# Performance work log

Measured on AMD Instinct MI355X. Metric: run time of the kernel, lower is better.

## Reference

```python
import jax, jax.numpy as jnp
import numpy as np

N_NODES = 50000


def gcn_conv(x, W, b, row, col, num_nodes):
    """PyG-style GCNConv: out = D^{-1/2}(A+I)D^{-1/2} (x @ W) + b.

    row/col already include self-loops. x: [N, Fin], W: [Fin, Fout].
    """
    h = x @ W  # [N, Fout]
    deg = jax.ops.segment_sum(jnp.ones_like(col, dtype=h.dtype), col,
                              num_segments=num_nodes)  # in-degree incl. self-loop
    dinv = jnp.where(deg > 0, jax.lax.rsqrt(deg), 0.0)
    norm = dinv[row] * dinv[col]  # [E]
    msgs = h[row] * norm[:, None]  # gather + scale, [E, Fout]
    out = jax.ops.segment_sum(msgs, col, num_segments=num_nodes)  # scatter-add
    return out + b


def setup_inputs() -> dict:
    key = jax.random.key(0)
    k1, k2, k3, k4 = jax.random.split(key, 4)
    Fin, Fh, Fout = 128, 128, 64
    E = 800000
    x = jax.random.normal(k1, (N_NODES, Fin), dtype=jnp.float32)
    edge_index = jax.random.randint(k2, (2, E), 0, N_NODES, dtype=jnp.int64)
    # Glorot-ish init for weights
    W1 = jax.random.normal(k3, (Fin, Fh), dtype=jnp.float32) / np.sqrt(Fin)
    b1 = jnp.zeros((Fh,), dtype=jnp.float32)
    W2 = jax.random.normal(k4, (Fh, Fout), dtype=jnp.float32) / np.sqrt(Fh)
    b2 = jnp.zeros((Fout,), dtype=jnp.float32)
    return {"x": x, "edge_index": edge_index, "W1": W1, "b1": b1,
            "W2": W2, "b2": b2}


def reference(x, edge_index, W1, b1, W2, b2):
    n = x.shape[0]
    # add self-loops once (shared by both conv layers)
    loops = jnp.arange(n, dtype=edge_index.dtype)
    row = jnp.concatenate([edge_index[0], loops])
    col = jnp.concatenate([edge_index[1], loops])
    h = jax.nn.relu(gcn_conv(x, W1, b1, row, col, n))
    # dropout(p=0.5) is identity in eval mode (self.training == False)
    return gcn_conv(h, W2, b2, row, col, n)
```

## Files before the change

### kernel.cpp

```cpp
#include <hip/hip_runtime.h>


constexpr int KD = 128;
constexpr int CHUNK = 2048;
constexpr int BCAP = 6144;

using short8  = __attribute__((ext_vector_type(8))) short;
using float4v = __attribute__((ext_vector_type(4))) float;
using uint4v  = __attribute__((ext_vector_type(4))) unsigned int;


__device__ __forceinline__ unsigned short f2bf(float f) {
    unsigned int u = __float_as_uint(f);
    u = (u + 0x7fffu + ((u >> 16) & 1u)) >> 16;
    return (unsigned short)u;
}

__device__ __forceinline__ float2 bfpair(unsigned int u) {
    float2 f;
    f.x = __uint_as_float(u << 16);
    f.y = __uint_as_float(u & 0xffff0000u);
    return f;
}

__device__ __forceinline__ unsigned int packbf(float x, float y) {
    return (unsigned int)f2bf(x) | ((unsigned int)f2bf(y) << 16);
}

__device__ __forceinline__ void bfsplit(float x, unsigned short& h, unsigned short& l) {
    h = f2bf(x);
    float fh = __uint_as_float((unsigned int)h << 16);
    l = f2bf(x - fh);
}

__global__ __launch_bounds__(256) void scatter_setup(
        const int* __restrict__ row, const int* __restrict__ col,
        int* gcur, unsigned int* __restrict__ bpack, int E, int NBS,
        const float* __restrict__ W1, unsigned short* __restrict__ Wth1,
        unsigned short* __restrict__ Wtl1,
        const float* __restrict__ W2, unsigned short* __restrict__ Wth2,
        unsigned short* __restrict__ Wtl2) {
    __shared__ int lh[256];
    __shared__ int lbase[256];

    if ((int)blockIdx.x >= NBS) {
        int id = ((int)blockIdx.x - NBS) * 256 + threadIdx.x;
        unsigned short h, l;
        if (id < 16384) {
            int k = id >> 7, n = id & 127;
            bfsplit(W1[id], h, l);
            Wth1[n * KD + k] = h;
            Wtl1[n * KD + k] = l;
        } else {
            int id2 = id - 16384;
            int k = id2 >> 6, n = id2 & 63;
            bfsplit(W2[id2], h, l);
            Wth2[n * KD + k] = h;
            Wtl2[n * KD + k] = l;
        }
        return;
    }

    lh[threadIdx.x] = 0;
    __syncthreads();
    int base = (int)blockIdx.x * CHUNK;
#pragma unroll
    for (int r = 0; r < CHUNK / 256; ++r) {
        int e = base + r * 256 + threadIdx.x;
        if (e < E) atomicAdd(&lh[col[e] >> 8], 1);
    }
    __syncthreads();
    int c0 = lh[threadIdx.x];
    lbase[threadIdx.x] = c0 ? (threadIdx.x * BCAP + atomicAdd(&gcur[threadIdx.x], c0)) : 0;
    __syncthreads();
    lh[threadIdx.x] = 0;
    __syncthreads();
#pragma unroll
    for (int r = 0; r < CHUNK / 256; ++r) {
        int e = base + r * 256 + threadIdx.x;
        if (e < E) {
            int c = col[e];
            int b = c >> 8;
            int slot = lbase[b] + atomicAdd(&lh[b], 1);
            bpack[slot] = ((unsigned int)row[e] << 16) | (unsigned int)c;
        }
    }
}

__global__ __launch_bounds__(256) void csr_and_gemm1(
        const unsigned int* __restrict__ bpack, const int* __restrict__ gcur,
        int* __restrict__ rowptrS, float* __restrict__ dinv,
        unsigned short* __restrict__ srow, int N, int E, int NBUCKET,
        const float* __restrict__ X,
        const unsigned short* __restrict__ Wth,
        const unsigned short* __restrict__ Wtl,
        unsigned short* __restrict__ G) {
    __shared__ int s[256];
    __shared__ int lh[1024];
    __shared__ int lcur[1024];
    __shared__ int sh_bstart;

    if ((int)blockIdx.x < NBUCKET) {
        int b = blockIdx.x;
        int t = threadIdx.x;
        int cntb = gcur[t];
        s[t] = cntb;
        __syncthreads();
        for (int off = 1; off < 256; off <<= 1) {
            int tv = (t >= off) ? s[t - off] : 0;
            __syncthreads();
            s[t] += tv;
            __syncthreads();
        }
        if (t == b) sh_bstart = s[t] - cntb;
        if (b == 0 && t == 0) rowptrS[4 * N] = E;
#pragma unroll
        for (int k = 0; k < 4; ++k) lh[t * 4 + k] = 0;
        __syncthreads();
        int bstart = sh_bstart;
        int nE = gcur[b];
        int base = b * BCAP;
        for (int i = t; i < nE; i += 256) {
            unsigned int p = bpack[base + i];
            atomicAdd(&lh[(p & 255) * 4 + (p >> 30)], 1);
        }
        __syncthreads();
        int e0 = lh[t * 4], e1 = lh[t * 4 + 1], e2 = lh[t * 4 + 2], e3 = lh[t * 4 + 3];
        int v = e0 + e1 + e2 + e3;
        s[t] = v;
        __syncthreads();
        for (int off = 1; off < 256; off <<= 1) {
            int tv = (t >= off) ? s[t - off] : 0;
            __syncthreads();
            s[t] += tv;
            __syncthreads();
        }
        int myStart = bstart + s[t] - v;
        int node = (b << 8) + t;
        if (node < N) {
            rowptrS[node * 4 + 0] = myStart;
            rowptrS[node * 4 + 1] = myStart + e0;
            rowptrS[node * 4 + 2] = myStart + e0 + e1;
            rowptrS[node * 4 + 3] = myStart + e0 + e1 + e2;
            dinv[node] = rsqrtf(1.0f + (float)v);
        }
        lcur[t * 4 + 0] = myStart;
        lcur[t * 4 + 1] = myStart + e0;
        lcur[t * 4 + 2] = myStart + e0 + e1;
        lcur[t * 4 + 3] = myStart + e0 + e1 + e2;
        __syncthreads();
        for (int i = t; i < nE; i += 256) {
            unsigned int p = bpack[base + i];
            int slot = atomicAdd(&lcur[(p & 255) * 4 + (p >> 30)], 1);
            srow[slot] = (unsigned short)(p >> 16);
        }
    } else {
        constexpr int FOUT = 128, NT = 8;
        int wave = threadIdx.x >> 6;
        int lane = threadIdx.x & 63;
        int row0 = (((int)blockIdx.x - NBUCKET) * 4 + wave) * 16;
        if (row0 >= N) return;
        int m = lane & 15;
        int quad = lane >> 4;

        float4v acc[NT];
#pragma unroll
        for (int ct = 0; ct < NT; ++ct) acc[ct] = (float4v){0.f, 0.f, 0.f, 0.f};

        const float* xrow = X + (size_t)(row0 + m) * KD + quad * 8;

#pragma unroll
        for (int ks = 0; ks < 4; ++ks) {
            float4 xa = *(const float4*)(xrow + ks * 32);
            float4 xb = *(const float4*)(xrow + ks * 32 + 4);
            float xs[8] = {xa.x, xa.y, xa.z, xa.w, xb.x, xb.y, xb.z, xb.w};
            short8 ah, al;
#pragma unroll
            for (int j = 0; j < 8; ++j) {
                unsigned short h, l;
                bfsplit(xs[j], h, l);
                ah[j] = (short)h;
                al[j] = (short)l;
            }
            int koff = ks * 32 + quad * 8;
#pragma unroll
            for (int ct = 0; ct < NT; ++ct) {
                short8 bh = *(const short8*)(Wth + (size_t)(ct * 16 + m) * KD + koff);
                short8 bl = *(const short8*)(Wtl + (size_t)(ct * 16 + m) * KD + koff);
                acc[ct] = __builtin_amdgcn_mfma_f32_16x16x32_bf16(ah, bh, acc[ct], 0, 0, 0);
                acc[ct] = __builtin_amdgcn_mfma_f32_16x16x32_bf16(al, bh, acc[ct], 0, 0, 0);
                acc[ct] = __builtin_amdgcn_mfma_f32_16x16x32_bf16(ah, bl, acc[ct], 0, 0, 0);
            }
        }

#pragma unroll
        for (int r = 0; r < 4; ++r) {
            int row = row0 + quad * 4 + r;
#pragma unroll
            for (int ct = 0; ct < NT; ++ct) {
                G[(size_t)row * FOUT + ct * 16 + m] = f2bf(acc[ct][r]);
            }
        }
    }
}

__global__ __launch_bounds__(256) void gather128_gemm2(
        const int* __restrict__ rowptrS,
        const unsigned short* __restrict__ srow,
        const unsigned int* __restrict__ G,
        const float* __restrict__ dinv,
        const float* __restrict__ bias,
        const unsigned short* __restrict__ Wth,
        const unsigned short* __restrict__ Wtl,
        unsigned short* __restrict__ G2,
        int N, int E) {
    __shared__ unsigned int lhs[16 * 64];
    __shared__ float ldinv[16];

    int lane = threadIdx.x & 63;
    int l16 = threadIdx.x & 15;
    int q = threadIdx.x >> 4;
    int node = (int)blockIdx.x * 16 + q;
    bool valid = node < N;
    int nc = valid ? node : 0;
    int beg = rowptrS[nc * 4];
    int end = rowptrS[nc * 4 + 4];
    int deg = valid ? (end - beg) : 0;
    float dn = dinv[nc];
    if (l16 == 0) ldinv[q] = dn;

    const uint4v* Gv = (const uint4v*)G;

    uint4v s0 = Gv[(size_t)nc * 16 + l16];
    float ac[8];
    {
        float2 v0 = bfpair(s0[0]), v1 = bfpair(s0[1]);
        float2 v2 = bfpair(s0[2]), v3 = bfpair(s0[3]);
        ac[0] = v0.x * dn; ac[1] = v0.y * dn;
        ac[2] = v1.x * dn; ac[3] = v1.y * dn;
        ac[4] = v2.x * dn; ac[5] = v2.y * dn;
        ac[6] = v3.x * dn; ac[7] = v3.y * dn;
    }

    int dm = max(deg, __shfl_xor(deg, 16));
    dm = max(dm, __shfl_xor(dm, 32));

    for (int w = 0; w < dm; w += 16) {
        int li = w + l16;
        li = (li < deg) ? li : (deg > 0 ? deg - 1 : 0);
        li += beg;
        li = (li < E) ? li : (E - 1);
        int rv = (int)srow[li];
        float dv = dinv[rv];
        int lim = dm - w;
        for (int g = 0; g < 16 && g < lim; g += 8) {
            uint4v u[8];
            float dr[8];
#pragma unroll
            for (int j = 0; j < 8; ++j) {
                int src = (lane & 48) | (g + j);
                int r = __shfl(rv, src);
                dr[j] = __shfl(dv, src);
                u[j] = Gv[(size_t)r * 16 + l16];
            }
            float sa[8] = {0.f, 0.f, 0.f, 0.f, 0.f, 0.f, 0.f, 0.f};
#pragma unroll
            for (int j = 0; j < 8; ++j) {
                bool ok = (w + g + j) < deg;
#pragma unroll
                for (int c = 0; c < 4; ++c) {
                    unsigned int uv = ok ? u[j][c] : 0u;
                    float2 v = bfpair(uv);
                    sa[2 * c]     = fmaf(dr[j], v.x, sa[2 * c]);
                    sa[2 * c + 1] = fmaf(dr[j], v.y, sa[2 * c + 1]);
                }
            }
#pragma unroll
            for (int c = 0; c < 8; ++c) ac[c] += sa[c];
        }
    }

    {
        float4 bv0 = ((const float4*)bias)[l16 * 2];
        float4 bv1 = ((const float4*)bias)[l16 * 2 + 1];
        float o[8];
        o[0] = ac[0] * dn + bv0.x; o[1] = ac[1] * dn + bv0.y;
        o[2] = ac[2] * dn + bv0.z; o[3] = ac[3] * dn + bv0.w;
        o[4] = ac[4] * dn + bv1.x; o[5] = ac[5] * dn + bv1.y;
        o[6] = ac[6] * dn + bv1.z; o[7] = ac[7] * dn + bv1.w;
#pragma unroll
        for (int c = 0; c < 8; ++c) o[c] = fmaxf(o[c], 0.f);
        int lb = q * 64 + l16 * 4;
        lhs[lb + 0] = packbf(o[0], o[1]);
        lhs[lb + 1] = packbf(o[2], o[3]);
        lhs[lb + 2] = packbf(o[4], o[5]);
        lhs[lb + 3] = packbf(o[6], o[7]);
    }
    __syncthreads();

    int ct = threadIdx.x >> 6;
    int m = lane & 15;
    int quad = lane >> 4;

    float4v acc = (float4v){0.f, 0.f, 0.f, 0.f};
#pragma unroll
    for (int ks = 0; ks < 4; ++ks) {
        short8 a = *(const short8*)&lhs[m * 64 + ks * 16 + quad * 4];
        int koff = ks * 32 + quad * 8;
        short8 bh = *(const short8*)(Wth + (size_t)(ct * 16 + m) * KD + koff);
        short8 bl = *(const short8*)(Wtl + (size_t)(ct * 16 + m) * KD + koff);
        acc = __builtin_amdgcn_mfma_f32_16x16x32_bf16(a, bh, acc, 0, 0, 0);
        acc = __builtin_amdgcn_mfma_f32_16x16x32_bf16(a, bl, acc, 0, 0, 0);
    }

#pragma unroll
    for (int r = 0; r < 4; ++r) {
        int rr = quad * 4 + r;
        int gnode = (int)blockIdx.x * 16 + rr;
        if (gnode < N) {
            G2[(size_t)gnode * 64 + ct * 16 + m] = f2bf(acc[r] * ldinv[rr]);
        }
    }
}

template <bool RELU>
__global__ __launch_bounds__(256) void gather64(const int* __restrict__ rowptrS,
                                                const unsigned short* __restrict__ srow,
                                                const unsigned int* __restrict__ G,
                                                const float* __restrict__ dinv,
                                                const float* __restrict__ bias,
                                                float* __restrict__ O, int N, int E) {
    int tid = blockIdx.x * 256 + (int)threadIdx.x;
    int node = tid >> 4;
    int lane = threadIdx.x & 63;
    int l16 = lane & 15;
    bool valid = node < N;
    int nc = valid ? node : (N - 1);
    int beg = rowptrS[nc * 4];
    int end = rowptrS[nc * 4 + 4];
    int deg = valid ? (end - beg) : 0;

    uint2 s0 = ((const uint2*)G)[(size_t)nc * 16 + l16];
    float2 p0 = bfpair(s0.x), p1 = bfpair(s0.y);
    float ax = p0.x, ay = p0.y, az = p1.x, aw = p1.y;

    int dm = max(deg, __shfl_xor(deg, 16));
    dm = max(dm, __shfl_xor(dm, 32));

    for (int w = 0; w < dm; w += 16) {
        int li = w + l16;
        li = (li < deg) ? li : (deg > 0 ? deg - 1 : 0);
        li += beg;
        li = (li < E) ? li : (E - 1);
        int rv = (int)srow[li];
        int lim = dm - w;
        for (int g = 0; g < 16 && g < lim; g += 8) {
            uint2 u[8];
#pragma unroll
            for (int j = 0; j < 8; ++j) {
                int src = (lane & 48) | (g + j);
                int r = __shfl(rv, src);
                u[j] = ((const uint2*)G)[(size_t)r * 16 + l16];
            }
            float sx = 0.f, sy = 0.f, sz = 0.f, sw = 0.f;
#pragma unroll
            for (int j = 0; j < 8; ++j) {
                bool ok = (w + g + j) < deg;
                unsigned int ux = ok ? u[j].x : 0u;
                unsigned int uy = ok ? u[j].y : 0u;
                float2 v0 = bfpair(ux), v1 = bfpair(uy);
                sx += v0.x; sy += v0.y; sz += v1.x; sw += v1.y;
            }
            ax += sx; ay += sy; az += sz; aw += sw;
        }
    }
    if (!valid) return;
    float s = dinv[nc];
    float4 bv = ((const float4*)bias)[l16];
    float ox = ax * s + bv.x;
    float oy = ay * s + bv.y;
    float oz = az * s + bv.z;
    float ow = aw * s + bv.w;
    if (RELU) {
        ox = fmaxf(ox, 0.f); oy = fmaxf(oy, 0.f);
        oz = fmaxf(oz, 0.f); ow = fmaxf(ow, 0.f);
    }
    float4v o = {ox, oy, oz, ow};
    __builtin_nontemporal_store(o, (float4v*)O + (size_t)nc * 16 + l16);
}

extern "C" void kernel_launch(void* const* d_in, const int* in_sizes, int n_in,
                              void* d_out, int out_size, void* d_ws, size_t ws_size,
                              hipStream_t stream) {
    const float* x  = (const float*)d_in[0];
    const int*   ei = (const int*)d_in[1];
    const float* W1 = (const float*)d_in[2];
    const float* b1 = (const float*)d_in[3];
    const float* W2 = (const float*)d_in[4];
    const float* b2 = (const float*)d_in[5];
    float* out = (float*)d_out;

    int N = in_sizes[0] / 128;
    int E = in_sizes[1] / 2;
    const int* row = ei;
    const int* col = ei + E;

    char* ws = (char*)d_ws;
    float* dinv    = (float*)(ws + 0x000000);
    int*   rowptrS = (int*)  (ws + 0x080000);
    int*   gcur    = (int*)  (ws + 0x150000);
    unsigned short* srow = (unsigned short*)(ws + 0x160000);
    unsigned short* g1 = (unsigned short*)(ws + 0x440000);
    unsigned short* wth1 = (unsigned short*)(ws + 0x10C0000);
    unsigned short* wtl1 = (unsigned short*)(ws + 0x10D0000);
    unsigned short* wth2 = (unsigned short*)(ws + 0x10E0000);
    unsigned short* wtl2 = (unsigned short*)(ws + 0x10F0000);
    unsigned int* bpack = (unsigned int*)(ws + 0x1200000);
    unsigned short* g2 = (unsigned short*)(ws + 0x2C00000);

    int NB_BKT  = (E + CHUNK - 1) / CHUNK;
    int NBUCKET = (N + 255) / 256;
    int NB_GEMM1 = (N + 63) / 64;
    int NB_SETUP = 96;

    hipMemsetAsync(gcur, 0, 256 * sizeof(int), stream);
    scatter_setup<<<NB_BKT + NB_SETUP, 256, 0, stream>>>(
        row, col, gcur, bpack, E, NB_BKT, W1, wth1, wtl1, W2, wth2, wtl2);
    csr_and_gemm1<<<NBUCKET + NB_GEMM1, 256, 0, stream>>>(
        bpack, gcur, rowptrS, dinv, srow, N, E, NBUCKET, x, wth1, wtl1, g1);

    int nb;
    nb = (N + 15) / 16;
    gather128_gemm2<<<nb, 256, 0, stream>>>(rowptrS, srow, (const unsigned int*)g1,
                                            dinv, b1, wth2, wtl2, g2, N, E);

    nb = (N + 15) / 16;
    gather64<false><<<nb, 256, 0, stream>>>(rowptrS, srow, (const unsigned int*)g2,
                                            dinv, b2, out, N, E);
}
```

Before: 183.4 us.

## Fuse all GCN stages into one cooperative persistent kernel with grid syncs

Replaces the memset and four separate kernel launches with one cooperative kernel of 1024 persistent blocks. The blocks loop over the virtual block ranges of each stage, with grid.sync between stages. This removes per-launch overhead and the inter-kernel gaps, but adds grid-wide barrier cost and a fixed grid size that may limit occupancy or load balance. The old multi-launch path is kept as a fallback if the cooperative launch fails.

```diff
diff --git a/kernel.cpp b/kernel.cpp
--- a/kernel.cpp
+++ b/kernel.cpp
@@ -1,9 +1,13 @@
 #include <hip/hip_runtime.h>
+#include <hip/hip_cooperative_groups.h>
+
+namespace cg = cooperative_groups;
 
 
 constexpr int KD = 128;
 constexpr int CHUNK = 2048;
 constexpr int BCAP = 6144;
+constexpr int GRID_COOP = 1024;
 
 using short8  = __attribute__((ext_vector_type(8))) short;
 using float4v = __attribute__((ext_vector_type(4))) float;
@@ -32,6 +36,358 @@
     float fh = __uint_as_float((unsigned int)h << 16);
     l = f2bf(x - fh);
 }
+
+struct KP {
+    const int* row; const int* col;
+    const float* X; const float* W1; const float* b1;
+    const float* W2; const float* b2;
+    float* out;
+    int* gcur; unsigned int* bpack; int* rowptrS; float* dinv;
+    unsigned short* srow; unsigned short* g1;
+    unsigned short* wth1; unsigned short* wtl1;
+    unsigned short* wth2; unsigned short* wtl2;
+    unsigned short* g2;
+    int N, E, NBS, NB1, NBUCKET, NB2, NB3, NB4;
+};
+
+__global__ __launch_bounds__(256, 4) void gcn_fused(KP p) {
+    cg::grid_group grid = cg::this_grid();
+
+    __shared__ int s_s[256];
+    __shared__ int s_lh[1024];
+    __shared__ int s_lcur[1024];
+    __shared__ int s_b;
+    __shared__ unsigned int s_lhs[16 * 64];
+    __shared__ float s_ldinv[16];
+
+    const int t = threadIdx.x;
+    const int lane = t & 63;
+
+    if (blockIdx.x == 0) p.gcur[t] = 0;
+    grid.sync();
+
+    for (int vb = blockIdx.x; vb < p.NB1; vb += gridDim.x) {
+        if (vb >= p.NBS) {
+            int id = (vb - p.NBS) * 256 + t;
+            unsigned short h, l;
+            if (id < 16384) {
+                int k = id >> 7, n = id & 127;
+                bfsplit(p.W1[id], h, l);
+                p.wth1[n * KD + k] = h;
+                p.wtl1[n * KD + k] = l;
+            } else {
+                int id2 = id - 16384;
+                int k = id2 >> 6, n = id2 & 63;
+                bfsplit(p.W2[id2], h, l);
+                p.wth2[n * KD + k] = h;
+                p.wtl2[n * KD + k] = l;
+            }
+        } else {
+            int* lh = s_lh;
+            int* lbase = s_lcur;
+            lh[t] = 0;
+            __syncthreads();
+            int base = vb * CHUNK;
+#pragma unroll
+            for (int r = 0; r < CHUNK / 256; ++r) {
+                int e = base + r * 256 + t;
+                if (e < p.E) atomicAdd(&lh[p.col[e] >> 8], 1);
+            }
+            __syncthreads();
+            int c0 = lh[t];
+            lbase[t] = c0 ? (t * BCAP + atomicAdd(&p.gcur[t], c0)) : 0;
+            __syncthreads();
+            lh[t] = 0;
+            __syncthreads();
+#pragma unroll
+            for (int r = 0; r < CHUNK / 256; ++r) {
+                int e = base + r * 256 + t;
+                if (e < p.E) {
+                    int c = p.col[e];
+                    int b = c >> 8;
+                    int slot = lbase[b] + atomicAdd(&lh[b], 1);
+                    p.bpack[slot] = ((unsigned int)p.row[e] << 16) | (unsigned int)c;
+                }
+            }
+            __syncthreads();
+        }
+    }
+    grid.sync();
+
+    for (int vb = blockIdx.x; vb < p.NB2; vb += gridDim.x) {
+        if (vb < p.NBUCKET) {
+            int b = vb;
+            int cntb = p.gcur[t];
+            s_s[t] = cntb;
+            __syncthreads();
+            for (int off = 1; off < 256; off <<= 1) {
+                int tv = (t >= off) ? s_s[t - off] : 0;
+                __syncthreads();
+                s_s[t] += tv;
+                __syncthreads();
+            }
+            if (t == b) s_b = s_s[t] - cntb;
+            if (b == 0 && t == 0) p.rowptrS[4 * p.N] = p.E;
+#pragma unroll
+            for (int k = 0; k < 4; ++k) s_lh[t * 4 + k] = 0;
+            __syncthreads();
+            int bstart = s_b;
+            int nE = p.gcur[b];
+            int base = b * BCAP;
+            for (int i = t; i < nE; i += 256) {
+                unsigned int pk = p.bpack[base + i];
+                atomicAdd(&s_lh[(pk & 255) * 4 + (pk >> 30)], 1);
+            }
+            __syncthreads();
+            int e0 = s_lh[t * 4], e1 = s_lh[t * 4 + 1];
+            int e2 = s_lh[t * 4 + 2], e3 = s_lh[t * 4 + 3];
+            int v = e0 + e1 + e2 + e3;
+            s_s[t] = v;
+            __syncthreads();
+            for (int off = 1; off < 256; off <<= 1) {
+                int tv = (t >= off) ? s_s[t - off] : 0;
+                __syncthreads();
+                s_s[t] += tv;
+                __syncthreads();
+            }
+            int myStart = bstart + s_s[t] - v;
+            int node = (b << 8) + t;
+            if (node < p.N) {
+                p.rowptrS[node * 4 + 0] = myStart;
+                p.rowptrS[node * 4 + 1] = myStart + e0;
+                p.rowptrS[node * 4 + 2] = myStart + e0 + e1;
+                p.rowptrS[node * 4 + 3] = myStart + e0 + e1 + e2;
+                p.dinv[node] = rsqrtf(1.0f + (float)v);
+            }
+            s_lcur[t * 4 + 0] = myStart;
+            s_lcur[t * 4 + 1] = myStart + e0;
+            s_lcur[t * 4 + 2] = myStart + e0 + e1;
+            s_lcur[t * 4 + 3] = myStart + e0 + e1 + e2;
+            __syncthreads();
+            for (int i = t; i < nE; i += 256) {
+                unsigned int pk = p.bpack[base + i];
+                int slot = atomicAdd(&s_lcur[(pk & 255) * 4 + (pk >> 30)], 1);
+                p.srow[slot] = (unsigned short)(pk >> 16);
+            }
+            __syncthreads();
+        } else {
+            constexpr int FOUT = 128, NT = 8;
+            int wave = t >> 6;
+            int row0 = ((vb - p.NBUCKET) * 4 + wave) * 16;
+            if (row0 < p.N) {
+                int m = lane & 15;
+                int quad = lane >> 4;
+
+                float4v acc[NT];
+#pragma unroll
+                for (int ct = 0; ct < NT; ++ct) acc[ct] = (float4v){0.f, 0.f, 0.f, 0.f};
+
+                const float* xrow = p.X + (size_t)(row0 + m) * KD + quad * 8;
+
+#pragma unroll
+                for (int ks = 0; ks < 4; ++ks) {
+                    float4 xa = *(const float4*)(xrow + ks * 32);
+                    float4 xb = *(const float4*)(xrow + ks * 32 + 4);
+                    float xs[8] = {xa.x, xa.y, xa.z, xa.w, xb.x, xb.y, xb.z, xb.w};
+                    short8 ah, al;
+#pragma unroll
+                    for (int j = 0; j < 8; ++j) {
+                        unsigned short h, l;
+                        bfsplit(xs[j], h, l);
+                        ah[j] = (short)h;
+                        al[j] = (short)l;
+                    }
+                    int koff = ks * 32 + quad * 8;
+#pragma unroll
+                    for (int ct = 0; ct < NT; ++ct) {
+                        short8 bh = *(const short8*)(p.wth1 + (size_t)(ct * 16 + m) * KD + koff);
+                        short8 bl = *(const short8*)(p.wtl1 + (size_t)(ct * 16 + m) * KD + koff);
+                        acc[ct] = __builtin_amdgcn_mfma_f32_16x16x32_bf16(ah, bh, acc[ct], 0, 0, 0);
+                        acc[ct] = __builtin_amdgcn_mfma_f32_16x16x32_bf16(al, bh, acc[ct], 0, 0, 0);
+                        acc[ct] = __builtin_amdgcn_mfma_f32_16x16x32_bf16(ah, bl, acc[ct], 0, 0, 0);
+                    }
+                }
+
+#pragma unroll
+                for (int r = 0; r < 4; ++r) {
+                    int row = row0 + quad * 4 + r;
+#pragma unroll
+                    for (int ct = 0; ct < NT; ++ct) {
+                        p.g1[(size_t)row * FOUT + ct * 16 + m] = f2bf(acc[ct][r]);
+                    }
+                }
+            }
+        }
+    }
+    grid.sync();
+
+    for (int vb = blockIdx.x; vb < p.NB3; vb += gridDim.x) {
+        int l16 = t & 15;
+        int q = t >> 4;
+        int node = vb * 16 + q;
+        bool valid = node < p.N;
+        int nc = valid ? node : 0;
+        int beg = p.rowptrS[nc * 4];
+        int end = p.rowptrS[nc * 4 + 4];
+        int deg = valid ? (end - beg) : 0;
+        float dn = p.dinv[nc];
+        if (l16 == 0) s_ldinv[q] = dn;
+
+        const uint4v* Gv = (const uint4v*)(const void*)p.g1;
+
+        uint4v s0 = Gv[(size_t)nc * 16 + l16];
+        float ac[8];
+        {
+            float2 v0 = bfpair(s0[0]), v1 = bfpair(s0[1]);
+            float2 v2 = bfpair(s0[2]), v3 = bfpair(s0[3]);
+            ac[0] = v0.x * dn; ac[1] = v0.y * dn;
+            ac[2] = v1.x * dn; ac[3] = v1.y * dn;
+            ac[4] = v2.x * dn; ac[5] = v2.y * dn;
+            ac[6] = v3.x * dn; ac[7] = v3.y * dn;
+        }
+
+        int dm = max(deg, __shfl_xor(deg, 16));
+        dm = max(dm, __shfl_xor(dm, 32));
+
+        for (int w = 0; w < dm; w += 16) {
+            int li = w + l16;
+            li = (li < deg) ? li : (deg > 0 ? deg - 1 : 0);
+            li += beg;
+            li = (li < p.E) ? li : (p.E - 1);
+            int rv = (int)p.srow[li];
+            float dv = p.dinv[rv];
+            int lim = dm - w;
+            for (int g = 0; g < 16 && g < lim; g += 8) {
+                uint4v u[8];
+                float dr[8];
+#pragma unroll
+                for (int j = 0; j < 8; ++j) {
+                    int src = (lane & 48) | (g + j);
+                    int r = __shfl(rv, src);
+                    dr[j] = __shfl(dv, src);
+                    u[j] = Gv[(size_t)r * 16 + l16];
+                }
+                float sa[8] = {0.f, 0.f, 0.f, 0.f, 0.f, 0.f, 0.f, 0.f};
+#pragma unroll
+                for (int j = 0; j < 8; ++j) {
+                    bool ok = (w + g + j) < deg;
+#pragma unroll
+                    for (int c = 0; c < 4; ++c) {
+                        unsigned int uv = ok ? u[j][c] : 0u;
+                        float2 v = bfpair(uv);
+                        sa[2 * c]     = fmaf(dr[j], v.x, sa[2 * c]);
+                        sa[2 * c + 1] = fmaf(dr[j], v.y, sa[2 * c + 1]);
+                    }
+                }
+#pragma unroll
+                for (int c = 0; c < 8; ++c) ac[c] += sa[c];
+            }
+        }
+
+        {
+            float4 bv0 = ((const float4*)p.b1)[l16 * 2];
+            float4 bv1 = ((const float4*)p.b1)[l16 * 2 + 1];
+            float o[8];
+            o[0] = ac[0] * dn + bv0.x; o[1] = ac[1] * dn + bv0.y;
+            o[2] = ac[2] * dn + bv0.z; o[3] = ac[3] * dn + bv0.w;
+            o[4] = ac[4] * dn + bv1.x; o[5] = ac[5] * dn + bv1.y;
+            o[6] = ac[6] * dn + bv1.z; o[7] = ac[7] * dn + bv1.w;
+#pragma unroll
+            for (int c = 0; c < 8; ++c) o[c] = fmaxf(o[c], 0.f);
+            int lb = q * 64 + l16 * 4;
+            s_lhs[lb + 0] = packbf(o[0], o[1]);
+            s_lhs[lb + 1] = packbf(o[2], o[3]);
+            s_lhs[lb + 2] = packbf(o[4], o[5]);
+            s_lhs[lb + 3] = packbf(o[6], o[7]);
+        }
+        __syncthreads();
+
+        {
+            int ct = t >> 6;
+            int m = lane & 15;
+            int quad = lane >> 4;
+
+            float4v acc = (float4v){0.f, 0.f, 0.f, 0.f};
+#pragma unroll
+            for (int ks = 0; ks < 4; ++ks) {
+                short8 a = *(const short8*)&s_lhs[m * 64 + ks * 16 + quad * 4];
+                int koff = ks * 32 + quad * 8;
+                short8 bh = *(const short8*)(p.wth2 + (size_t)(ct * 16 + m) * KD + koff);
+                short8 bl = *(const short8*)(p.wtl2 + (size_t)(ct * 16 + m) * KD + koff);
+                acc = __builtin_amdgcn_mfma_f32_16x16x32_bf16(a, bh, acc, 0, 0, 0);
+                acc = __builtin_amdgcn_mfma_f32_16x16x32_bf16(a, bl, acc, 0, 0, 0);
+            }
+
+#pragma unroll
+            for (int r = 0; r < 4; ++r) {
+                int rr = quad * 4 + r;
+                int gnode = vb * 16 + rr;
+                if (gnode < p.N) {
+                    p.g2[(size_t)gnode * 64 + ct * 16 + m] = f2bf(acc[r] * s_ldinv[rr]);
+                }
+            }
+        }
+        __syncthreads();
+    }
+    grid.sync();
+
+    for (int vb = blockIdx.x; vb < p.NB4; vb += gridDim.x) {
+        int tid = vb * 256 + t;
+        int node = tid >> 4;
+        int l16 = lane & 15;
+        bool valid = node < p.N;
+        int nc = valid ? node : (p.N - 1);
+        int beg = p.rowptrS[nc * 4];
+        int end = p.rowptrS[nc * 4 + 4];
+        int deg = valid ? (end - beg) : 0;
+
+        uint2 s0 = ((const uint2*)(const void*)p.g2)[(size_t)nc * 16 + l16];
+        float2 p0 = bfpair(s0.x), p1 = bfpair(s0.y);
+        float ax = p0.x, ay = p0.y, az = p1.x, aw = p1.y;
+
+        int dm = max(deg, __shfl_xor(deg, 16));
+        dm = max(dm, __shfl_xor(dm, 32));
+
+        for (int w = 0; w < dm; w += 16) {
+            int li = w + l16;
+            li = (li < deg) ? li : (deg > 0 ? deg - 1 : 0);
+            li += beg;
+            li = (li < p.E) ? li : (p.E - 1);
+            int rv = (int)p.srow[li];
+            int lim = dm - w;
+            for (int g = 0; g < 16 && g < lim; g += 8) {
+                uint2 u[8];
+#pragma unroll
+                for (int j = 0; j < 8; ++j) {
+                    int src = (lane & 48) | (g + j);
+                    int r = __shfl(rv, src);
+                    u[j] = ((const uint2*)(const void*)p.g2)[(size_t)r * 16 + l16];
+                }
+                float sx = 0.f, sy = 0.f, sz = 0.f, sw = 0.f;
+#pragma unroll
+                for (int j = 0; j < 8; ++j) {
+                    bool ok = (w + g + j) < deg;
+                    unsigned int ux = ok ? u[j].x : 0u;
+                    unsigned int uy = ok ? u[j].y : 0u;
+                    float2 v0 = bfpair(ux), v1 = bfpair(uy);
+                    sx += v0.x; sy += v0.y; sz += v1.x; sw += v1.y;
+                }
+                ax += sx; ay += sy; az += sz; aw += sw;
+            }
+        }
+        if (valid) {
+            float s = p.dinv[nc];
+            float4 bv = ((const float4*)p.b2)[l16];
+            float ox = ax * s + bv.x;
+            float oy = ay * s + bv.y;
+            float oz = az * s + bv.z;
+            float ow = aw * s + bv.w;
+            float4v o = {ox, oy, oz, ow};
+            __builtin_nontemporal_store(o, (float4v*)p.out + (size_t)nc * 16 + l16);
+        }
+    }
+}
+
 
 __global__ __launch_bounds__(256) void scatter_setup(
         const int* __restrict__ row, const int* __restrict__ col,
@@ -422,19 +778,35 @@
     int NBUCKET = (N + 255) / 256;
     int NB_GEMM1 = (N + 63) / 64;
     int NB_SETUP = 96;
-
-    hipMemsetAsync(gcur, 0, 256 * sizeof(int), stream);
-    scatter_setup<<<NB_BKT + NB_SETUP, 256, 0, stream>>>(
-        row, col, gcur, bpack, E, NB_BKT, W1, wth1, wtl1, W2, wth2, wtl2);
-    csr_and_gemm1<<<NBUCKET + NB_GEMM1, 256, 0, stream>>>(
-        bpack, gcur, rowptrS, dinv, srow, N, E, NBUCKET, x, wth1, wtl1, g1);
-
-    int nb;
-    nb = (N + 15) / 16;
-    gather128_gemm2<<<nb, 256, 0, stream>>>(rowptrS, srow, (const unsigned int*)g1,
-                                            dinv, b1, wth2, wtl2, g2, N, E);
-
-    nb = (N + 15) / 16;
-    gather64<false><<<nb, 256, 0, stream>>>(rowptrS, srow, (const unsigned int*)g2,
-                                            dinv, b2, out, N, E);
-}
+    int NB_G = (N + 15) / 16;
+
+    KP p;
+    p.row = row; p.col = col;
+    p.X = x; p.W1 = W1; p.b1 = b1; p.W2 = W2; p.b2 = b2;
+    p.out = out;
+    p.gcur = gcur; p.bpack = bpack; p.rowptrS = rowptrS; p.dinv = dinv;
+    p.srow = srow; p.g1 = g1;
+    p.wth1 = wth1; p.wtl1 = wtl1; p.wth2 = wth2; p.wtl2 = wtl2;
+    p.g2 = g2;
+    p.N = N; p.E = E;
+    p.NBS = NB_BKT; p.NB1 = NB_BKT + NB_SETUP;
+    p.NBUCKET = NBUCKET; p.NB2 = NBUCKET + NB_GEMM1;
+    p.NB3 = NB_G; p.NB4 = NB_G;
+
+    void* args[] = {&p};
+    hipError_t err = hipLaunchCooperativeKernel(
+        (const void*)gcn_fused, dim3(GRID_COOP), dim3(256), args, 0, stream);
+
+    if (err != hipSuccess) {
+        (void)hipGetLastError();
+        hipMemsetAsync(gcur, 0, 256 * sizeof(int), stream);
+        scatter_setup<<<NB_BKT + NB_SETUP, 256, 0, stream>>>(
+            row, col, gcur, bpack, E, NB_BKT, W1, wth1, wtl1, W2, wth2, wtl2);
+        csr_and_gemm1<<<NBUCKET + NB_GEMM1, 256, 0, stream>>>(
+            bpack, gcur, rowptrS, dinv, srow, N, E, NBUCKET, x, wth1, wtl1, g1);
+        gather128_gemm2<<<NB_G, 256, 0, stream>>>(
+            rowptrS, srow, (const unsigned int*)g1, dinv, b1, wth2, wtl2, g2, N, E);
+        gather64<false><<<NB_G, 256, 0, stream>>>(
+            rowptrS, srow, (const unsigned int*)g2, dinv, b2, out, N, E);
+    }
+}
```

New measurement: 714.0 us. +289.3%, slower.

## Split gathers into feature-column chunks and unfuse second GEMM into own kernel

Applied to the files above, without the earlier changes.

The fused gather+GEMM2 kernel is split in two. A column-chunked gather (4 chunks of 32 features, blockIdx selects tile and chunk) writes the relu'd hidden layer to a workspace buffer, and a separate MFMA GEMM kernel then produces the dinv-scaled layer-2 features. The final 64-wide gather is likewise split into 2 column chunks. Chunking shrinks each kernel's working set of gathered rows so that more of it fits in cache. The cost is redundant CSR index and dinv loads per chunk, narrower 4-byte gathers, an extra kernel launch, and an extra round trip of the hidden layer through memory.

```diff
diff --git a/kernel.cpp b/kernel.cpp
--- a/kernel.cpp
+++ b/kernel.cpp
@@ -7,7 +7,6 @@
 
 using short8  = __attribute__((ext_vector_type(8))) short;
 using float4v = __attribute__((ext_vector_type(4))) float;
-using uint4v  = __attribute__((ext_vector_type(4))) unsigned int;
 
 
 __device__ __forceinline__ unsigned short f2bf(float f) {
@@ -204,43 +203,30 @@
     }
 }
 
-__global__ __launch_bounds__(256) void gather128_gemm2(
+__global__ __launch_bounds__(256) void gather128_chunk(
         const int* __restrict__ rowptrS,
         const unsigned short* __restrict__ srow,
         const unsigned int* __restrict__ G,
         const float* __restrict__ dinv,
         const float* __restrict__ bias,
-        const unsigned short* __restrict__ Wth,
-        const unsigned short* __restrict__ Wtl,
-        unsigned short* __restrict__ G2,
-        int N, int E) {
-    __shared__ unsigned int lhs[16 * 64];
-    __shared__ float ldinv[16];
-
+        unsigned int* __restrict__ H2,
+        int N, int E, int NTILE) {
+    int tile = (int)blockIdx.x % NTILE;
+    int c    = (int)blockIdx.x / NTILE;
     int lane = threadIdx.x & 63;
-    int l16 = threadIdx.x & 15;
-    int q = threadIdx.x >> 4;
-    int node = (int)blockIdx.x * 16 + q;
+    int l16  = threadIdx.x & 15;
+    int q    = threadIdx.x >> 4;
+    int node = tile * 16 + q;
     bool valid = node < N;
     int nc = valid ? node : 0;
     int beg = rowptrS[nc * 4];
     int end = rowptrS[nc * 4 + 4];
     int deg = valid ? (end - beg) : 0;
     float dn = dinv[nc];
-    if (l16 == 0) ldinv[q] = dn;
-
-    const uint4v* Gv = (const uint4v*)G;
-
-    uint4v s0 = Gv[(size_t)nc * 16 + l16];
-    float ac[8];
-    {
-        float2 v0 = bfpair(s0[0]), v1 = bfpair(s0[1]);
-        float2 v2 = bfpair(s0[2]), v3 = bfpair(s0[3]);
-        ac[0] = v0.x * dn; ac[1] = v0.y * dn;
-        ac[2] = v1.x * dn; ac[3] = v1.y * dn;
-        ac[4] = v2.x * dn; ac[5] = v2.y * dn;
-        ac[6] = v3.x * dn; ac[7] = v3.y * dn;
-    }
+
+    unsigned int su = G[(size_t)nc * 64 + c * 16 + l16];
+    float2 sv = bfpair(su);
+    float a0 = sv.x * dn, a1 = sv.y * dn;
 
     int dm = max(deg, __shfl_xor(deg, 16));
     dm = max(dm, __shfl_xor(dm, 32));
@@ -253,96 +239,100 @@
         int rv = (int)srow[li];
         float dv = dinv[rv];
         int lim = dm - w;
-        for (int g = 0; g < 16 && g < lim; g += 8) {
-            uint4v u[8];
-            float dr[8];
-#pragma unroll
-            for (int j = 0; j < 8; ++j) {
+        for (int g = 0; g < 16 && g < lim; g += 4) {
+            unsigned int u[4];
+            float dr[4];
+#pragma unroll
+            for (int j = 0; j < 4; ++j) {
                 int src = (lane & 48) | (g + j);
                 int r = __shfl(rv, src);
                 dr[j] = __shfl(dv, src);
-                u[j] = Gv[(size_t)r * 16 + l16];
-            }
-            float sa[8] = {0.f, 0.f, 0.f, 0.f, 0.f, 0.f, 0.f, 0.f};
-#pragma unroll
-            for (int j = 0; j < 8; ++j) {
+                u[j] = G[(size_t)r * 64 + c * 16 + l16];
+            }
+            float s0 = 0.f, s1 = 0.f;
+#pragma unroll
+            for (int j = 0; j < 4; ++j) {
                 bool ok = (w + g + j) < deg;
-#pragma unroll
-                for (int c = 0; c < 4; ++c) {
-                    unsigned int uv = ok ? u[j][c] : 0u;
-                    float2 v = bfpair(uv);
-                    sa[2 * c]     = fmaf(dr[j], v.x, sa[2 * c]);
-                    sa[2 * c + 1] = fmaf(dr[j], v.y, sa[2 * c + 1]);
-                }
-            }
-#pragma unroll
-            for (int c = 0; c < 8; ++c) ac[c] += sa[c];
-        }
-    }
-
-    {
-        float4 bv0 = ((const float4*)bias)[l16 * 2];
-        float4 bv1 = ((const float4*)bias)[l16 * 2 + 1];
-        float o[8];
-        o[0] = ac[0] * dn + bv0.x; o[1] = ac[1] * dn + bv0.y;
-        o[2] = ac[2] * dn + bv0.z; o[3] = ac[3] * dn + bv0.w;
-        o[4] = ac[4] * dn + bv1.x; o[5] = ac[5] * dn + bv1.y;
-        o[6] = ac[6] * dn + bv1.z; o[7] = ac[7] * dn + bv1.w;
-#pragma unroll
-        for (int c = 0; c < 8; ++c) o[c] = fmaxf(o[c], 0.f);
-        int lb = q * 64 + l16 * 4;
-        lhs[lb + 0] = packbf(o[0], o[1]);
-        lhs[lb + 1] = packbf(o[2], o[3]);
-        lhs[lb + 2] = packbf(o[4], o[5]);
-        lhs[lb + 3] = packbf(o[6], o[7]);
-    }
-    __syncthreads();
-
-    int ct = threadIdx.x >> 6;
+                unsigned int uv = ok ? u[j] : 0u;
+                float2 v = bfpair(uv);
+                s0 = fmaf(dr[j], v.x, s0);
+                s1 = fmaf(dr[j], v.y, s1);
+            }
+            a0 += s0; a1 += s1;
+        }
+    }
+    if (!valid) return;
+    float2 bv = ((const float2*)bias)[c * 16 + l16];
+    float o0 = fmaxf(a0 * dn + bv.x, 0.f);
+    float o1 = fmaxf(a1 * dn + bv.y, 0.f);
+    H2[(size_t)nc * 64 + c * 16 + l16] = packbf(o0, o1);
+}
+
+__global__ __launch_bounds__(256) void gemm_mfma2(const unsigned short* __restrict__ H,
+                                                  const unsigned short* __restrict__ Wth,
+                                                  const unsigned short* __restrict__ Wtl,
+                                                  const float* __restrict__ dinv,
+                                                  unsigned short* __restrict__ G, int N) {
+    constexpr int FOUT = 64, NT = 4;
+    int wave = threadIdx.x >> 6;
+    int lane = threadIdx.x & 63;
+    int row0 = (blockIdx.x * 4 + wave) * 16;
+    if (row0 >= N) return;
     int m = lane & 15;
     int quad = lane >> 4;
 
-    float4v acc = (float4v){0.f, 0.f, 0.f, 0.f};
+    float4v acc[NT];
+#pragma unroll
+    for (int ct = 0; ct < NT; ++ct) acc[ct] = (float4v){0.f, 0.f, 0.f, 0.f};
+
+    const unsigned short* hrow = H + (size_t)(row0 + m) * KD + quad * 8;
+
 #pragma unroll
     for (int ks = 0; ks < 4; ++ks) {
-        short8 a = *(const short8*)&lhs[m * 64 + ks * 16 + quad * 4];
+        short8 a = *(const short8*)(hrow + ks * 32);
         int koff = ks * 32 + quad * 8;
-        short8 bh = *(const short8*)(Wth + (size_t)(ct * 16 + m) * KD + koff);
-        short8 bl = *(const short8*)(Wtl + (size_t)(ct * 16 + m) * KD + koff);
-        acc = __builtin_amdgcn_mfma_f32_16x16x32_bf16(a, bh, acc, 0, 0, 0);
-        acc = __builtin_amdgcn_mfma_f32_16x16x32_bf16(a, bl, acc, 0, 0, 0);
+#pragma unroll
+        for (int ct = 0; ct < NT; ++ct) {
+            short8 bh = *(const short8*)(Wth + (size_t)(ct * 16 + m) * KD + koff);
+            short8 bl = *(const short8*)(Wtl + (size_t)(ct * 16 + m) * KD + koff);
+            acc[ct] = __builtin_amdgcn_mfma_f32_16x16x32_bf16(a, bh, acc[ct], 0, 0, 0);
+            acc[ct] = __builtin_amdgcn_mfma_f32_16x16x32_bf16(a, bl, acc[ct], 0, 0, 0);
+        }
     }
 
 #pragma unroll
     for (int r = 0; r < 4; ++r) {
-        int rr = quad * 4 + r;
-        int gnode = (int)blockIdx.x * 16 + rr;
-        if (gnode < N) {
-            G2[(size_t)gnode * 64 + ct * 16 + m] = f2bf(acc[r] * ldinv[rr]);
-        }
-    }
-}
-
-template <bool RELU>
-__global__ __launch_bounds__(256) void gather64(const int* __restrict__ rowptrS,
-                                                const unsigned short* __restrict__ srow,
-                                                const unsigned int* __restrict__ G,
-                                                const float* __restrict__ dinv,
-                                                const float* __restrict__ bias,
-                                                float* __restrict__ O, int N, int E) {
-    int tid = blockIdx.x * 256 + (int)threadIdx.x;
-    int node = tid >> 4;
+        int row = row0 + quad * 4 + r;
+        float s = dinv[row];
+#pragma unroll
+        for (int ct = 0; ct < 4; ++ct) {
+            G[(size_t)row * FOUT + ct * 16 + m] = f2bf(acc[ct][r] * s);
+        }
+    }
+}
+
+__global__ __launch_bounds__(256) void gather64_chunk(
+        const int* __restrict__ rowptrS,
+        const unsigned short* __restrict__ srow,
+        const unsigned int* __restrict__ G,
+        const float* __restrict__ dinv,
+        const float* __restrict__ bias,
+        float* __restrict__ O, int N, int E, int NTILE) {
+    int tile = (int)blockIdx.x % NTILE;
+    int c    = (int)blockIdx.x / NTILE;
     int lane = threadIdx.x & 63;
-    int l16 = lane & 15;
+    int l16  = threadIdx.x & 15;
+    int q    = threadIdx.x >> 4;
+    int node = tile * 16 + q;
     bool valid = node < N;
     int nc = valid ? node : (N - 1);
     int beg = rowptrS[nc * 4];
     int end = rowptrS[nc * 4 + 4];
     int deg = valid ? (end - beg) : 0;
 
-    uint2 s0 = ((const uint2*)G)[(size_t)nc * 16 + l16];
-    float2 p0 = bfpair(s0.x), p1 = bfpair(s0.y);
-    float ax = p0.x, ay = p0.y, az = p1.x, aw = p1.y;
+    unsigned int su = G[(size_t)nc * 32 + c * 16 + l16];
+    float2 sv = bfpair(su);
+    float a0 = sv.x, a1 = sv.y;
 
     int dm = max(deg, __shfl_xor(deg, 16));
     dm = max(dm, __shfl_xor(dm, 32));
@@ -355,38 +345,32 @@
         int rv = (int)srow[li];
         int lim = dm - w;
         for (int g = 0; g < 16 && g < lim; g += 8) {
-            uint2 u[8];
+            unsigned int u[8];
 #pragma unroll
             for (int j = 0; j < 8; ++j) {
                 int src = (lane & 48) | (g + j);
                 int r = __shfl(rv, src);
-                u[j] = ((const uint2*)G)[(size_t)r * 16 + l16];
-            }
-            float sx = 0.f, sy = 0.f, sz = 0.f, sw = 0.f;
+                u[j] = G[(size_t)r * 32 + c * 16 + l16];
+            }
+            float s0 = 0.f, s1 = 0.f;
 #pragma unroll
             for (int j = 0; j < 8; ++j) {
                 bool ok = (w + g + j) < deg;
-                unsigned int ux = ok ? u[j].x : 0u;
-                unsigned int uy = ok ? u[j].y : 0u;
-                float2 v0 = bfpair(ux), v1 = bfpair(uy);
-                sx += v0.x; sy += v0.y; sz += v1.x; sw += v1.y;
-            }
-            ax += sx; ay += sy; az += sz; aw += sw;
+                unsigned int uv = ok ? u[j] : 0u;
+                float2 v = bfpair(uv);
+                s0 += v.x; s1 += v.y;
+            }
+            a0 += s0; a1 += s1;
         }
     }
     if (!valid) return;
     float s = dinv[nc];
-    float4 bv = ((const float4*)bias)[l16];
-    float ox = ax * s + bv.x;
-    float oy = ay * s + bv.y;
-    float oz = az * s + bv.z;
-    float ow = aw * s + bv.w;
-    if (RELU) {
-        ox = fmaxf(ox, 0.f); oy = fmaxf(oy, 0.f);
-        oz = fmaxf(oz, 0.f); ow = fmaxf(ow, 0.f);
-    }
-    float4v o = {ox, oy, oz, ow};
-    __builtin_nontemporal_store(o, (float4v*)O + (size_t)nc * 16 + l16);
+    float2 bv = ((const float2*)bias)[c * 16 + l16];
+    float2 o = make_float2(a0 * s + bv.x, a1 * s + bv.y);
+    unsigned long long pv;
+    __builtin_memcpy(&pv, &o, 8);
+    __builtin_nontemporal_store(pv,
+        (unsigned long long*)&((float2*)O)[(size_t)nc * 32 + c * 16 + l16]);
 }
 
 extern "C" void kernel_launch(void* const* d_in, const int* in_sizes, int n_in,
@@ -416,12 +400,14 @@
     unsigned short* wth2 = (unsigned short*)(ws + 0x10E0000);
     unsigned short* wtl2 = (unsigned short*)(ws + 0x10F0000);
     unsigned int* bpack = (unsigned int*)(ws + 0x1200000);
+    unsigned short* h2 = (unsigned short*)(ws + 0x1200000);
     unsigned short* g2 = (unsigned short*)(ws + 0x2C00000);
 
     int NB_BKT  = (E + CHUNK - 1) / CHUNK;
     int NBUCKET = (N + 255) / 256;
     int NB_GEMM1 = (N + 63) / 64;
     int NB_SETUP = 96;
+    int NTILE = (N + 15) / 16;
 
     hipMemsetAsync(gcur, 0, 256 * sizeof(int), stream);
     scatter_setup<<<NB_BKT + NB_SETUP, 256, 0, stream>>>(
@@ -429,12 +415,12 @@
     csr_and_gemm1<<<NBUCKET + NB_GEMM1, 256, 0, stream>>>(
         bpack, gcur, rowptrS, dinv, srow, N, E, NBUCKET, x, wth1, wtl1, g1);
 
-    int nb;
-    nb = (N + 15) / 16;
-    gather128_gemm2<<<nb, 256, 0, stream>>>(rowptrS, srow, (const unsigned int*)g1,
-                                            dinv, b1, wth2, wtl2, g2, N, E);
-
-    nb = (N + 15) / 16;
-    gather64<false><<<nb, 256, 0, stream>>>(rowptrS, srow, (const unsigned int*)g2,
-                                            dinv, b2, out, N, E);
-}
+    gather128_chunk<<<4 * NTILE, 256, 0, stream>>>(
+        rowptrS, srow, (const unsigned int*)g1, dinv, b1,
+        (unsigned int*)h2, N, E, NTILE);
+
+    gemm_mfma2<<<NB_GEMM1, 256, 0, stream>>>(h2, wth2, wtl2, dinv, g2, N);
+
+    gather64_chunk<<<2 * NTILE, 256, 0, stream>>>(
+        rowptrS, srow, (const unsigned int*)g2, dinv, b2, out, N, E, NTILE);
+}
```

Result: slower. 215.1 us (+17.3%).
